# Optimization experiments

Measured on AMD Instinct MI355X. Metric: run time of the kernel, lower is better.

The kernel has to match this reference:

```python
import jax, jax.numpy as jnp
import numpy as np

B, N, D, E_PER, NT, ET, L = 32, 64, 128, 512, 32, 16, 6
E = B * E_PER


def _ln(y, g, b, eps=1e-5):
    m = jnp.mean(y, -1, keepdims=True)
    v = jnp.mean((y - m) ** 2, -1, keepdims=True)
    return (y - m) * jax.lax.rsqrt(v + eps) * g + b


def setup_inputs() -> dict:
    key = jax.random.key(0)
    ks = jax.random.split(key, 40)
    x = jax.random.randint(ks[0], (B * N,), 0, NT)
    src = jax.random.randint(ks[1], (E,), 0, N)
    dst = jax.random.randint(ks[2], (E,), 0, N)
    off = jnp.repeat(jnp.arange(B) * N, E_PER)
    edge_index = jnp.stack([src + off, dst + off])
    edge_attr = jax.random.randint(ks[3], (E,), 0, ET)
    t = jax.random.uniform(ks[4], (B,))

    def lin(k, fi, fo):
        return jax.random.normal(k, (fi, fo), jnp.float32) / np.sqrt(fi).astype(np.float32)

    inp = {
        'x': x, 'edge_index': edge_index, 'edge_attr': edge_attr, 't': t,
        'node_emb': (jax.random.normal(ks[5], (NT, D)) * 0.02).at[0].set(0.0),
        'edge_emb': (jax.random.normal(ks[6], (ET, D)) * 0.02).at[0].set(0.0),
        'temb_W1': lin(ks[7], 1, D), 'temb_b1': jnp.zeros(D),
        'temb_W2': lin(ks[8], D, D), 'temb_b2': jnp.zeros(D),
        'nin_W1': lin(ks[9], D, 2 * D), 'nin_b1': jnp.zeros(2 * D),
        'nin_W2': lin(ks[10], 2 * D, D), 'nin_b2': jnp.zeros(D),
        'ein_W1': lin(ks[11], D, 2 * D), 'ein_b1': jnp.zeros(2 * D),
        'ein_W2': lin(ks[12], 2 * D, D), 'ein_b2': jnp.zeros(D),
        'conv_W1': jax.random.normal(ks[13], (L, 3 * D, D)) / np.sqrt(3 * D).astype(np.float32),
        'conv_b1': jnp.zeros((L, D)),
        'conv_g1': jnp.ones((L, D)), 'conv_bt1': jnp.zeros((L, D)),
        'conv_W2': jax.random.normal(ks[14], (L, D, D)) / np.sqrt(D).astype(np.float32),
        'conv_b2': jnp.zeros((L, D)),
        'conv_g2': jnp.ones((L, D)), 'conv_bt2': jnp.zeros((L, D)),
        'mlp_W1': lin(ks[15], D, D), 'mlp_b1': jnp.zeros(D),
        'mlp_W2': lin(ks[16], D, D), 'mlp_b2': jnp.zeros(D),
        'fn_W1': lin(ks[17], D, 2 * D), 'fn_b1': jnp.zeros(2 * D),
        'fn_W2': lin(ks[18], 2 * D, D), 'fn_b2': jnp.zeros(D),
    }
    return inp


def reference(x, edge_index, edge_attr, t, node_emb, edge_emb,
              temb_W1, temb_b1, temb_W2, temb_b2,
              nin_W1, nin_b1, nin_W2, nin_b2,
              ein_W1, ein_b1, ein_W2, ein_b2,
              conv_W1, conv_b1, conv_g1, conv_bt1,
              conv_W2, conv_b2, conv_g2, conv_bt2,
              mlp_W1, mlp_b1, mlp_W2, mlp_b2,
              fn_W1, fn_b1, fn_W2, fn_b2):
    silu, relu = jax.nn.silu, jax.nn.relu
    # encoders
    h = node_emb[x]                                   # (B*N, D)
    e = edge_emb[edge_attr]                           # (E, D)
    h = relu(h @ nin_W1 + nin_b1) @ nin_W2 + nin_b2
    e = relu(e @ ein_W1 + ein_b1) @ ein_W2 + ein_b2
    # densify (to_dense_adj sums duplicate edges)
    g = edge_index[0] // N
    u = edge_index[0] % N
    v = edge_index[1] % N
    adj = jnp.zeros((B, N, N, D), h.dtype).at[g, u, v].add(e)
    # time embedding scales adj
    tt = silu(silu(t[:, None] @ temb_W1 + temb_b1) @ temb_W2 + temb_b2)  # (B, D)
    X = adj * tt[:, None, None, :]
    A = X  # A fixed to initial masked tensor, X updated residually
    for l in range(L):
        X1 = jnp.einsum('bikd,bkjd->bijd', A, X)      # aggregate over dim 1
        X2 = jnp.einsum('bikd,bkjd->bijd', X, A)      # aggregate over dim 2
        y = jnp.concatenate([X, X1, X2], -1)          # (B,N,N,3D)
        y = relu(_ln(y @ conv_W1[l] + conv_b1[l], conv_g1[l], conv_bt1[l]))
        y = relu(_ln(y @ conv_W2[l] + conv_b2[l], conv_g2[l], conv_bt2[l]))
        X = X + y                                     # residual, samesparse add
    X = X + jnp.transpose(X, (0, 2, 1, 3))
    e_out = X[g, u, v]                                # (E, D) edge gather
    h2 = (silu(X @ mlp_W1 + mlp_b1) @ mlp_W2 + mlp_b2).mean(-2).reshape(B * N, D)
    node_out = relu(h2 @ fn_W1 + fn_b1) @ fn_W2 + fn_b2
    edge_out = relu(e_out @ fn_W1 + fn_b1) @ fn_W2 + fn_b2  # original uses final_layer_node for edges too
    graph_attr = node_out.reshape(B, N, -1).mean(1)   # global mean pool
    return node_out, edge_out, graph_attr
```

## Files before the change

kernel.cpp:

```cpp
#include <hip/hip_runtime.h>
#include <hip/hip_bf16.h>
#include <math.h>

#define NB 32
#define NNODE 64
#define DD 128
#define NSQ 4096
#define EDGES 16384
#define LAYERS 6

typedef __bf16 bf16x8 __attribute__((ext_vector_type(8)));
typedef float f32x4 __attribute__((ext_vector_type(4)));

typedef __attribute__((address_space(1))) const unsigned int g_u32;
typedef __attribute__((address_space(3))) unsigned int l_u32;
__device__ __forceinline__ void gll16(const void* g, void* l){
  __builtin_amdgcn_global_load_lds((g_u32*)g, (l_u32*)l, 16, 0, 0);
}

__device__ __forceinline__ float silu_f(float x){ return x / (1.f + __expf(-x)); }
__device__ __forceinline__ float bf2f(unsigned short h){
  union{unsigned int u; float f;} x; x.u = ((unsigned int)h)<<16; return x.f;
}
__device__ __forceinline__ uint4 addbf8(uint4 a, uint4 b){
  union { __bf16 h[8]; uint4 u; } A, B, O;
  A.u = a; B.u = b;
  #pragma unroll
  for (int e=0;e<8;e++) O.h[e] = (__bf16)((float)A.h[e] + (float)B.h[e]);
  return O.u;
}

__global__ void k_temb(const float* __restrict__ t, const float* __restrict__ W1,
                       const float* __restrict__ b1, const float* __restrict__ W2,
                       const float* __restrict__ b2, float* __restrict__ tt){
  int b = blockIdx.x, d = threadIdx.x;
  __shared__ float h[DD];
  float v = t[b]*W1[d] + b1[d];
  h[d] = silu_f(v);
  __syncthreads();
  float acc = b2[d];
  #pragma unroll 4
  for (int k=0;k<DD;k++) acc = fmaf(h[k], W2[k*DD+d], acc);
  tt[b*DD+d] = silu_f(acc);
}

__global__ void k_edgeenc(const float* __restrict__ emb, const float* __restrict__ W1,
                          const float* __restrict__ b1, const float* __restrict__ W2,
                          const float* __restrict__ b2, float* __restrict__ enc){
  int et = blockIdx.x, tid = threadIdx.x;
  __shared__ float e0[DD];
  __shared__ float hid[2*DD];
  if (tid < DD) e0[tid] = emb[et*DD + tid];
  __syncthreads();
  float a = b1[tid];
  for (int d2=0; d2<DD; d2++) a = fmaf(e0[d2], W1[d2*256 + tid], a);
  hid[tid] = fmaxf(a, 0.f);
  __syncthreads();
  if (tid < DD){
    float o = b2[tid];
    for (int k=0;k<256;k++) o = fmaf(hid[k], W2[k*DD + tid], o);
    enc[et*DD + tid] = o;
  }
}

__global__ void k_cnt(const int* __restrict__ ei, const int* __restrict__ attr,
                      unsigned int* __restrict__ cnt, int b0){
  int e = b0*512 + blockIdx.x*256 + threadIdx.x;
  int s = ei[e], dN = ei[EDGES+e];
  int g = (s>>6) - b0, u = s&63, v = dN&63;
  atomicAdd(&cnt[((size_t)g*4096 + v*64 + u)*16 + attr[e]], 1u);
}

__global__ __launch_bounds__(256) void k_expand(const unsigned int* __restrict__ cnt,
    const float* __restrict__ enc, const float* __restrict__ tt,
    __bf16* __restrict__ A_S, int b0){
  __shared__ float encs[16][128];
  __shared__ float ttl[128];
  __shared__ __bf16 tb[8][256];
  int g = blockIdx.x >> 4;
  int cell0 = (blockIdx.x & 15) << 8;
  int tid = threadIdx.x;
  for (int s = tid; s < 2048; s += 256) encs[s>>7][s&127] = enc[s];
  if (tid < 128) ttl[tid] = tt[(b0+g)*128 + tid];
  unsigned int c16[16];
  { const uint4* src = (const uint4*)(cnt + ((size_t)g*4096 + cell0 + tid)*16);
    uint4 a = src[0], b = src[1], c = src[2], d = src[3];
    c16[0]=a.x; c16[1]=a.y; c16[2]=a.z; c16[3]=a.w;
    c16[4]=b.x; c16[5]=b.y; c16[6]=b.z; c16[7]=b.w;
    c16[8]=c.x; c16[9]=c.y; c16[10]=c.z; c16[11]=c.w;
    c16[12]=d.x; c16[13]=d.y; c16[14]=d.z; c16[15]=d.w; }
  __syncthreads();
  for (int dc=0; dc<16; dc++){
    int d0 = dc*8;
    float vals[8] = {0.f,0.f,0.f,0.f,0.f,0.f,0.f,0.f};
    #pragma unroll
    for (int et=0; et<16; et++){
      unsigned int c = c16[et];
      if (c){
        float fc = (float)c;
        #pragma unroll
        for (int dd=0; dd<8; dd++) vals[dd] = fmaf(fc, encs[et][d0+dd], vals[dd]);
      }
    }
    #pragma unroll
    for (int dd=0; dd<8; dd++) tb[dd][tid] = (__bf16)(vals[dd]*ttl[d0+dd]);
    __syncthreads();
    { int dd = tid>>5, seg = tid&31;
      uint4 v = *(const uint4*)&tb[dd][seg*8];
      *(uint4*)(A_S + ((size_t)(g*128 + d0 + dd)<<12) + cell0 + seg*8) = v; }
    __syncthreads();
  }
}

__global__ __launch_bounds__(256) void k_wprep(const float* __restrict__ W1, const float* __restrict__ W2,
                                               const float* __restrict__ Wm, __bf16* __restrict__ WT){
  int b = blockIdx.x, t = threadIdx.x;
  const float* src; __bf16* dst; int K;
  if (b < 6){ src = W1 + (size_t)b*384*128; dst = WT + (size_t)b*49152; K = 384; }
  else if (b < 12){ src = W2 + (size_t)(b-6)*128*128; dst = WT + 294912 + (size_t)(b-6)*16384; K = 128; }
  else { src = Wm; dst = WT + 393216; K = 128; }
  __shared__ float L[64][129];
  for (int k0 = 0; k0 < K; k0 += 64){
    __syncthreads();
    int r = t>>2, c = (t&3)*32;
    #pragma unroll
    for (int e=0;e<32;e+=4){
      float4 x = *(const float4*)(src + (size_t)(k0+r)*128 + c + e);
      L[r][c+e]=x.x; L[r][c+e+1]=x.y; L[r][c+e+2]=x.z; L[r][c+e+3]=x.w;
    }
    __syncthreads();
    int fo = t>>1, kk = (t&1)*32;
    union { __bf16 h[32]; uint4 u[4]; } o;
    #pragma unroll
    for (int e=0;e<32;e++) o.h[e] = (__bf16)L[kk+e][fo];
    uint4* d4 = (uint4*)(dst + (size_t)fo*K + k0 + kk);
    d4[0]=o.u[0]; d4[1]=o.u[1]; d4[2]=o.u[2]; d4[3]=o.u[3];
  }
}

__global__ __launch_bounds__(256) void k_wprepfn(const float* __restrict__ W1, const float* __restrict__ W2,
                                                 __bf16* __restrict__ o1, __bf16* __restrict__ o2){
  int b = blockIdx.x, t = threadIdx.x;
  const float* src; __bf16* dst; int K, N, k0, n0;
  if (b < 8){ src = W1; dst = o1; K = 128; N = 256; k0 = (b>>2)*64; n0 = (b&3)*64; }
  else { int bb = b-8; src = W2; dst = o2; K = 256; N = 128; k0 = (bb>>1)*64; n0 = (bb&1)*64; }
  __shared__ float L[64][65];
  int r = t>>2, c4 = (t&3)*16;
  #pragma unroll
  for (int e=0;e<16;e+=4){
    float4 x = *(const float4*)(src + (size_t)(k0+r)*N + n0 + c4 + e);
    L[r][c4+e]=x.x; L[r][c4+e+1]=x.y; L[r][c4+e+2]=x.z; L[r][c4+e+3]=x.w;
  }
  __syncthreads();
  int n = t>>2, kc = (t&3)*16;
  union { __bf16 h[16]; uint4 u[2]; } o;
  #pragma unroll
  for (int e=0;e<16;e++) o.h[e] = (__bf16)L[kc+e][n];
  uint4* d4 = (uint4*)(dst + (size_t)(n0+n)*K + k0 + kc);
  d4[0]=o.u[0]; d4[1]=o.u[1];
}

__global__ __launch_bounds__(256) void k_einsum(const __bf16* __restrict__ As,
                                                const __bf16* __restrict__ Xs,
                                                __bf16* __restrict__ X1t, __bf16* __restrict__ X2t){
  __shared__ __bf16 S[8][4096];
  int tid = threadIdx.x;
  int w = tid>>6, lane = tid&63;
  size_t p0 = (size_t)blockIdx.x * 2;
  {
    int slot = (w<2) ? (2+w) : (4+w);
    const __bf16* srcp = ((w<2) ? As : Xs) + (p0 + (w&1))*4096;
    #pragma unroll
    for (int c8 = 0; c8 < 8; c8++){
      int row = c8*8 + (lane>>3);
      int ch  = (lane&7) ^ (row&7);
      gll16(srcp + row*64 + ch*8, (char*)&S[slot][0] + c8*1024);
    }
  }
  __syncthreads();
  {
    int q = tid>>6, v = tid&63;
    int ssl = (q<2) ? (2+q) : (4+q);
    int dsl = (q<2) ? q : (2+q);
    const unsigned char* sb = (const unsigned char*)S[ssl];
    unsigned char* db = (unsigned char*)S[dsl];
    #pragma unroll
    for (int uo=0; uo<8; uo++){
      union { __bf16 h[8]; uint4 u; } pk;
      #pragma unroll
      for (int e=0;e<8;e++){
        int u = uo*8+e;
        pk.h[e] = *(const __bf16*)(sb + u*128 + (((v>>3) ^ (u&7))<<4) + (v&7)*2);
      }
      *(uint4*)(db + v*128 + ((uo ^ (v&7))<<4)) = pk.u;
    }
  }
  __syncthreads();
  int pl = w>>1, pr = w&1;
  const __bf16* M  = pr ? S[4+pl] : S[0+pl];
  const __bf16* Bt = pr ? S[2+pl] : S[6+pl];
  f32x4 acc[4][4];
  #pragma unroll
  for (int a=0;a<4;a++)
    #pragma unroll
    for(int b=0;b<4;b++) acc[a][b] = (f32x4){0.f,0.f,0.f,0.f};
  int lr = lane&15, lq = lane>>4;
  #pragma unroll
  for (int ks=0;ks<2;ks++){
    bf16x8 af[4], bfr[4];
    #pragma unroll
    for (int mt=0;mt<4;mt++){ int r = mt*16+lr; af[mt] = *(const bf16x8*)&M[r*64 + (((ks*4+lq) ^ (r&7))<<3)]; }
    #pragma unroll
    for (int nt=0;nt<4;nt++){ int r = nt*16+lr; bfr[nt] = *(const bf16x8*)&Bt[r*64 + (((ks*4+lq) ^ (r&7))<<3)]; }
    #pragma unroll
    for (int mt=0;mt<4;mt++)
      #pragma unroll
      for (int nt=0;nt<4;nt++)
        acc[mt][nt] = __builtin_amdgcn_mfma_f32_16x16x32_bf16(af[mt], bfr[nt], acc[mt][nt], 0,0,0);
  }
  {
    int dslot = pr ? (4+pl) : pl;
    unsigned char* db = (unsigned char*)&S[dslot][0];
    #pragma unroll
    for (int mt=0;mt<4;mt++)
      #pragma unroll
      for (int nt=0;nt<4;nt++){
        int col = nt*16 + lr; int row0 = mt*16 + lq*4;
        union { __bf16 h[4]; uint2 u; } o;
        #pragma unroll
        for (int r=0;r<4;r++) o.h[r] = (__bf16)acc[mt][nt][r];
        int chunk = row0>>3;
        *(uint2*)(db + col*128 + ((chunk ^ (col&7))<<4) + (row0&7)*2) = o.u;
      }
  }
  __syncthreads();
  #pragma unroll
  for (int s4=0; s4<4; s4++){
    int slot = (s4<2) ? s4 : (2+s4);
    __bf16* dst = ((s4<2) ? X1t : X2t) + (p0 + (s4&1))*4096;
    const unsigned char* sb = (const unsigned char*)&S[slot][0];
    #pragma unroll
    for (int q=0;q<2;q++){
      int t2 = tid + q*256;
      int col = t2>>3, rc = t2&7;
      uint4 v = *(const uint4*)(sb + col*128 + ((rc ^ (col&7))<<4));
      *(uint4*)(dst + t2*8) = v;
    }
  }
}

__global__ __launch_bounds__(256) void k_layer(const __bf16* __restrict__ Xold,
    const __bf16* __restrict__ X1, const __bf16* __restrict__ X2,
    const __bf16* __restrict__ W1t, const __bf16* __restrict__ W2t,
    const float* __restrict__ b1v, const float* __restrict__ g1v, const float* __restrict__ bt1v,
    const float* __restrict__ b2v, const float* __restrict__ g2v, const float* __restrict__ bt2v,
    __bf16* __restrict__ Xnew){
  __shared__ __align__(16) unsigned char RG[32768];
  __shared__ float stats[2][128];
  __bf16* y1T = (__bf16*)RG;
  float (*redS)[128] = (float(*)[128])(RG + 16384);
  float (*redQ)[128] = (float(*)[128])(RG + 18432);
  int tid = threadIdx.x, w = tid>>6, lane = tid&63, lr = lane&15, lq = lane>>4;
  int colTile = blockIdx.x << 7;
  int bl = colTile >> 12;
  int colInB = colTile & 4095;
  int s_fi = tid>>3, s_o = tid&7;
  int r_col = tid>>1;

  f32x4 acc[2][8];
  #pragma unroll
  for (int a=0;a<2;a++)
    #pragma unroll
    for (int b=0;b<8;b++) acc[a][b] = (f32x4){0.f,0.f,0.f,0.f};

#define STAGE(ks, nb) { \
    int gfi = (ks)*32 + s_fi; \
    const __bf16* T = (gfi<128)? Xold : (gfi<256? X1 : X2); \
    int d = gfi & 127; \
    const uint4* src = (const uint4*)(T + ((size_t)(bl*128 + d)<<12) + colInB + s_o*16); \
    uint4 v0 = src[0], v1 = src[1]; \
    unsigned char* Nd = RG + (nb)*8192; \
    *(uint4*)(Nd + s_fi*256 + (((s_o*2+0) ^ (s_fi&15))<<4)) = v0; \
    *(uint4*)(Nd + s_fi*256 + (((s_o*2+1) ^ (s_fi&15))<<4)) = v1; \
  }

#define REPACK(nb) { \
    const unsigned char* Ns = RG + (nb)*8192; \
    unsigned char* Cd = RG + 16384 + (nb)*8192; \
    _Pragma("unroll") \
    for (int j=0;j<2;j++){ \
      int oct = (tid&1)*2 + j; \
      union { __bf16 h[8]; uint4 u; } pk; \
      _Pragma("unroll") \
      for (int e=0;e<8;e++){ \
        int fi = oct*8 + e; \
        pk.h[e] = *(const __bf16*)(Ns + fi*256 + (((r_col>>3) ^ (fi&15))<<4) + (r_col&7)*2); \
      } \
      *(uint4*)(Cd + r_col*64 + ((oct ^ (r_col&3))<<4)) = pk.u; \
    } \
  }

  STAGE(0, 0)
  STAGE(1, 1)
  __syncthreads();
  REPACK(0)
  __syncthreads();

  for (int k=0; k<11; k++){
    int cb = k&1, nb = cb^1;
    const unsigned char* Cc = RG + 16384 + cb*8192;
    bf16x8 af[2];
    #pragma unroll
    for (int mt=0;mt<2;mt++){
      int fo = w*32 + mt*16 + lr;
      af[mt] = *(const bf16x8*)(W1t + (size_t)fo*384 + k*32 + lq*8);
    }
    bf16x8 bfr[8];
    #pragma unroll
    for (int nt=0;nt<8;nt++){ int cr = nt*16+lr; bfr[nt] = *(const bf16x8*)(Cc + cr*64 + ((lq ^ (cr&3))<<4)); }
    #pragma unroll
    for (int mt=0;mt<2;mt++)
      #pragma unroll
      for (int nt=0;nt<8;nt++)
        acc[mt][nt] = __builtin_amdgcn_mfma_f32_16x16x32_bf16(af[mt], bfr[nt], acc[mt][nt], 0,0,0);
    REPACK(nb)
    if (k < 10) STAGE(k+2, cb)
    __syncthreads();
  }
  {
    const unsigned char* Cc = RG + 16384 + 8192;
    bf16x8 af[2];
    #pragma unroll
    for (int mt=0;mt<2;mt++){
      int fo = w*32 + mt*16 + lr;
      af[mt] = *(const bf16x8*)(W1t + (size_t)fo*384 + 11*32 + lq*8);
    }
    bf16x8 bfr[8];
    #pragma unroll
    for (int nt=0;nt<8;nt++){ int cr = nt*16+lr; bfr[nt] = *(const bf16x8*)(Cc + cr*64 + ((lq ^ (cr&3))<<4)); }
    #pragma unroll
    for (int mt=0;mt<2;mt++)
      #pragma unroll
      for (int nt=0;nt<8;nt++)
        acc[mt][nt] = __builtin_amdgcn_mfma_f32_16x16x32_bf16(af[mt], bfr[nt], acc[mt][nt], 0,0,0);
  }

  #pragma unroll
  for (int mt=0;mt<2;mt++){
    #pragma unroll
    for (int r=0;r<4;r++){
      float bv = b1v[w*32 + mt*16 + lq*4 + r];
      #pragma unroll
      for (int nt=0;nt<8;nt++) acc[mt][nt][r] += bv;
    }
  }
  {
    float cs[8], cq[8];
    #pragma unroll
    for (int nt=0;nt<8;nt++){ cs[nt]=0.f; cq[nt]=0.f; }
    #pragma unroll
    for (int mt=0;mt<2;mt++)
      #pragma unroll
      for (int nt=0;nt<8;nt++)
        #pragma unroll
        for (int r=0;r<4;r++){ float v = acc[mt][nt][r]; cs[nt] += v; cq[nt] = fmaf(v,v,cq[nt]); }
    #pragma unroll
    for (int nt=0;nt<8;nt++){
      cs[nt] += __shfl_xor(cs[nt], 16); cq[nt] += __shfl_xor(cq[nt], 16);
      cs[nt] += __shfl_xor(cs[nt], 32); cq[nt] += __shfl_xor(cq[nt], 32);
    }
    if (lq == 0){
      #pragma unroll
      for (int nt=0;nt<8;nt++){ redS[w][nt*16+lr] = cs[nt]; redQ[w][nt*16+lr] = cq[nt]; }
    }
  }
  __syncthreads();
  if (tid < 128){
    float S = redS[0][tid]+redS[1][tid]+redS[2][tid]+redS[3][tid];
    float Q = redQ[0][tid]+redQ[1][tid]+redQ[2][tid]+redQ[3][tid];
    float m = S*(1.f/128.f);
    float var = Q*(1.f/128.f) - m*m;
    stats[0][tid] = m; stats[1][tid] = rsqrtf(var + 1e-5f);
  }
  __syncthreads();
  #pragma unroll
  for (int mt=0;mt<2;mt++){
    int fo1b = w*32 + mt*16 + lq*4;
    float ga[4], be[4];
    #pragma unroll
    for (int r=0;r<4;r++){ ga[r] = g1v[fo1b+r]; be[r] = bt1v[fo1b+r]; }
    #pragma unroll
    for (int nt=0;nt<8;nt++){
      int col = nt*16 + lr;
      union { __bf16 h[4]; uint2 u; } o;
      #pragma unroll
      for (int r=0;r<4;r++){
        float xx = (acc[mt][nt][r] - stats[0][col]) * stats[1][col] * ga[r] + be[r];
        o.h[r] = (__bf16)fmaxf(xx, 0.f);
      }
      *(uint2*)&y1T[col*128 + (fo1b ^ ((col&15)<<3))] = o.u;
    }
  }
  __syncthreads();

  f32x4 acc2[2][8];
  #pragma unroll
  for (int a=0;a<2;a++)
    #pragma unroll
    for (int b=0;b<8;b++) acc2[a][b] = (f32x4){0.f,0.f,0.f,0.f};
  #pragma unroll
  for (int ks2=0; ks2<4; ks2++){
    bf16x8 af[2], bfr[8];
    #pragma unroll
    for (int mt=0;mt<2;mt++){
      int fo = w*32 + mt*16 + lr;
      af[mt] = *(const bf16x8*)(W2t + (size_t)fo*128 + ks2*32 + lq*8);
    }
    #pragma unroll
    for (int nt=0;nt<8;nt++){ int cr = nt*16+lr; bfr[nt] = *(const bf16x8*)&y1T[cr*128 + ((ks2*32 + lq*8) ^ ((cr&15)<<3))]; }
    #pragma unroll
    for (int mt=0;mt<2;mt++)
      #pragma unroll
      for (int nt=0;nt<8;nt++)
        acc2[mt][nt] = __builtin_amdgcn_mfma_f32_16x16x32_bf16(af[mt], bfr[nt], acc2[mt][nt], 0,0,0);
  }
  __syncthreads();

  #pragma unroll
  for (int mt=0;mt<2;mt++){
    #pragma unroll
    for (int r=0;r<4;r++){
      float bv = b2v[w*32 + mt*16 + lq*4 + r];
      #pragma unroll
      for (int nt=0;nt<8;nt++) acc2[mt][nt][r] += bv;
    }
  }
  {
    float cs[8], cq[8];
    #pragma unroll
    for (int nt=0;nt<8;nt++){ cs[nt]=0.f; cq[nt]=0.f; }
    #pragma unroll
    for (int mt=0;mt<2;mt++)
      #pragma unroll
      for (int nt=0;nt<8;nt++)
        #pragma unroll
        for (int r=0;r<4;r++){ float v = acc2[mt][nt][r]; cs[nt] += v; cq[nt] = fmaf(v,v,cq[nt]); }
    #pragma unroll
    for (int nt=0;nt<8;nt++){
      cs[nt] += __shfl_xor(cs[nt], 16); cq[nt] += __shfl_xor(cq[nt], 16);
      cs[nt] += __shfl_xor(cs[nt], 32); cq[nt] += __shfl_xor(cq[nt], 32);
    }
    if (lq == 0){
      #pragma unroll
      for (int nt=0;nt<8;nt++){ redS[w][nt*16+lr] = cs[nt]; redQ[w][nt*16+lr] = cq[nt]; }
    }
  }
  __syncthreads();
  if (tid < 128){
    float S = redS[0][tid]+redS[1][tid]+redS[2][tid]+redS[3][tid];
    float Q = redQ[0][tid]+redQ[1][tid]+redQ[2][tid]+redQ[3][tid];
    float m = S*(1.f/128.f);
    float var = Q*(1.f/128.f) - m*m;
    stats[0][tid] = m; stats[1][tid] = rsqrtf(var + 1e-5f);
  }
  __syncthreads();
  #pragma unroll
  for (int mt=0;mt<2;mt++){
    #pragma unroll
    for (int r=0;r<4;r++){
      int fo = w*32 + mt*16 + lq*4 + r;
      float ga = g2v[fo], be = bt2v[fo];
      size_t rowb = ((size_t)(bl*128 + fo)<<12) + colInB;
      #pragma unroll
      for (int nt=0;nt<8;nt++){
        int cp = nt*16 + lr;
        float xx = (acc2[mt][nt][r] - stats[0][cp]) * stats[1][cp] * ga + be;
        float o = fmaxf(xx, 0.f);
        float old = (float)Xold[rowb + cp];
        Xnew[rowb + cp] = (__bf16)(o + old);
      }
    }
  }
#undef STAGE
#undef REPACK
}

__global__ __launch_bounds__(256) void k_tonm(const __bf16* __restrict__ S, __bf16* __restrict__ NM){
  __shared__ unsigned short L[64][65];
  int b = blockIdx.x;
  int g = b >> 7, dh = (b>>6)&1, cc = b&63;
  int cell0 = cc*64, d0 = dh*64;
  int tid = threadIdx.x;
  int r = tid>>2, c = (tid&3)*16;
  union { unsigned short h[16]; uint4 u[2]; } in;
  const unsigned short* src = (const unsigned short*)S + ((size_t)(g*128 + d0 + r)<<12) + cell0 + c;
  in.u[0] = *(const uint4*)src;
  in.u[1] = *(const uint4*)(src + 8);
  #pragma unroll
  for (int e=0;e<16;e++) L[r][c+e] = in.h[e];
  __syncthreads();
  union { unsigned short h[16]; uint4 u[2]; } o;
  int cr = tid>>2, dc = (tid&3)*16;
  #pragma unroll
  for (int e=0;e<16;e++) o.h[e] = L[dc+e][cr];
  unsigned short* dst = (unsigned short*)NM + (size_t)(g*4096 + cell0 + cr)*128 + d0 + dc;
  *(uint4*)dst       = o.u[0];
  *(uint4*)(dst + 8) = o.u[1];
}

__global__ __launch_bounds__(256) void k_mlph(const __bf16* __restrict__ NM,
    const __bf16* __restrict__ Wt, const float* __restrict__ bias, __bf16* __restrict__ hid){
  __shared__ __align__(16) unsigned char WcB[8192];
  __shared__ __align__(16) unsigned char EcB[8192];
  __bf16* Wc = (__bf16*)WcB;
  unsigned char* Ec = EcB;
  int tid = threadIdx.x, w = tid>>6, lane = tid&63, lr = lane&15, lq = lane>>4;
  int g = blockIdx.x >> 5;
  int cellloc0 = (blockIdx.x & 31) << 7;
  size_t cellbase = ((size_t)g<<12) + cellloc0;
  int mh = w&1, nh = w>>1;
  f32x4 acc[4][4];
  #pragma unroll
  for (int a=0;a<4;a++)
    #pragma unroll
    for (int b=0;b<4;b++) acc[a][b] = (f32x4){0.f,0.f,0.f,0.f};
  for (int ks=0; ks<4; ks++){
    __syncthreads();
    { int fo = tid>>1, half = tid&1;
      const uint4* src = (const uint4*)(Wt + (size_t)fo*128 + ks*32 + half*16);
      uint4 v0 = src[0], v1 = src[1];
      *(uint4*)&Wc[fo*32 + (((half*2+0) ^ (fo&3))<<3)] = v0;
      *(uint4*)&Wc[fo*32 + (((half*2+1) ^ (fo&3))<<3)] = v1;
    }
    { int cell = tid>>1, half = tid&1;
      int cl = cellloc0 + cell;
      int v = cl>>6, u = cl&63;
      size_t cT = ((size_t)g<<12) + u*64 + v;
      const uint4* src  = (const uint4*)(NM + (cellbase + cell)*128 + ks*32 + half*16);
      const uint4* srcT = (const uint4*)(NM + cT*128 + ks*32 + half*16);
      uint4 v0 = addbf8(src[0], srcT[0]);
      uint4 v1 = addbf8(src[1], srcT[1]);
      *(uint4*)(Ec + cell*64 + (((half*2+0) ^ (cell&3))<<4)) = v0;
      *(uint4*)(Ec + cell*64 + (((half*2+1) ^ (cell&3))<<4)) = v1;
    }
    __syncthreads();
    bf16x8 af[4], bfr[4];
    #pragma unroll
    for (int mt=0;mt<4;mt++){ int cr = mh*64 + mt*16 + lr; af[mt] = *(const bf16x8*)(Ec + cr*64 + ((lq ^ (cr&3))<<4)); }
    #pragma unroll
    for (int nt=0;nt<4;nt++){ int fo = nh*64 + nt*16 + lr; bfr[nt] = *(const bf16x8*)&Wc[fo*32 + ((lq ^ (fo&3))<<3)]; }
    #pragma unroll
    for (int mt=0;mt<4;mt++)
      #pragma unroll
      for (int nt=0;nt<4;nt++)
        acc[mt][nt] = __builtin_amdgcn_mfma_f32_16x16x32_bf16(af[mt], bfr[nt], acc[mt][nt], 0,0,0);
  }
  #pragma unroll
  for (int mt=0;mt<4;mt++)
    #pragma unroll
    for (int r=0;r<4;r++){
      size_t cell = cellbase + mh*64 + mt*16 + lq*4 + r;
      #pragma unroll
      for (int nt=0;nt<4;nt++){
        int fo = nh*64 + nt*16 + lr;
        hid[cell*128 + fo] = (__bf16)silu_f(acc[mt][nt][r] + bias[fo]);
      }
    }
}

__global__ void k_ymean(const __bf16* __restrict__ hid, float* __restrict__ ym){
  __shared__ float red[256];
  int g = blockIdx.x >> 6, u = blockIdx.x & 63;
  int fo = threadIdx.x & 127, vh = threadIdx.x >> 7;
  const unsigned short* hu = (const unsigned short*)hid;
  float s = 0.f;
  for (int v = vh; v < 64; v += 2)
    s += bf2f(hu[((size_t)g*4096 + v*64 + u)*128 + fo]);
  red[threadIdx.x] = s;
  __syncthreads();
  if (vh == 0) ym[((size_t)g*64 + u)*128 + fo] = (red[fo] + red[128+fo]) * (1.f/64.f);
}

__global__ void k_h2(const float* __restrict__ ym, const float* __restrict__ W2,
                     const float* __restrict__ b2, float* __restrict__ h2){
  int row = blockIdx.x, fo = threadIdx.x;
  __shared__ float rr[128];
  rr[fo] = ym[(size_t)row*128 + fo];
  __syncthreads();
  float a = b2[fo];
  #pragma unroll 4
  for (int k=0;k<128;k++) a = fmaf(rr[k], W2[k*128+fo], a);
  h2[(size_t)row*128+fo] = a;
}

template<int GATHER>
__global__ __launch_bounds__(256) void k_fmlp(const __bf16* __restrict__ NM, const float* __restrict__ RWS,
    const int* __restrict__ ei,
    const __bf16* __restrict__ W1t, const float* __restrict__ b1,
    const __bf16* __restrict__ W2t, const float* __restrict__ b2,
    float* __restrict__ outp, int b0){
  __shared__ __align__(16) unsigned char RA[32768];
  __shared__ __align__(16) unsigned char RB[8192];
  __shared__ int cells[64];
  __shared__ int cellsT[64];
  __bf16* eo  = (__bf16*)RA;
  __bf16* Wc  = (__bf16*)(RA + 16384);
  __bf16* hid = (__bf16*)RA;
  __bf16* W2c = (__bf16*)RB;
  int tid = threadIdx.x, w = tid>>6, lane = tid&63, lr = lane&15, lq = lane>>4;
  int r0 = blockIdx.x*64;
  if (GATHER){
    if (tid < 64){
      int e = b0*512 + r0 + tid;
      int s = ei[e], dN = ei[EDGES+e];
      int g = (s>>6) - b0, u = s&63, v = dN&63;
      cells[tid]  = g*4096 + v*64 + u;
      cellsT[tid] = g*4096 + u*64 + v;
    }
    __syncthreads();
  }
  { int el = tid>>2, o4 = tid&3;
    if (GATHER){
      const unsigned short* src  = (const unsigned short*)NM + (size_t)cells[el]*128;
      const unsigned short* srcT = (const unsigned short*)NM + (size_t)cellsT[el]*128;
      #pragma unroll
      for (int j=0;j<4;j++){
        int ch = o4*4 + j;
        uint4 v = addbf8(*(const uint4*)(src + ch*8), *(const uint4*)(srcT + ch*8));
        *(uint4*)&eo[el*128 + ((ch*8) ^ ((el&15)*8))] = v;
      }
    } else {
      const float* src = RWS + (size_t)(r0 + el)*128;
      #pragma unroll
      for (int j=0;j<4;j++){
        int ch = o4*4 + j;
        union { __bf16 h[8]; uint4 u; } pk;
        #pragma unroll
        for (int e2=0;e2<8;e2++) pk.h[e2] = (__bf16)src[ch*8 + e2];
        *(uint4*)&eo[el*128 + ((ch*8) ^ ((el&15)*8))] = pk.u;
      }
    }
  }
  f32x4 acc[4][4];
  #pragma unroll
  for (int a=0;a<4;a++)
    #pragma unroll
    for (int b=0;b<4;b++) acc[a][b] = (f32x4){0.f,0.f,0.f,0.f};
  for (int ks=0; ks<4; ks++){
    if (ks) __syncthreads();
    { int fo = tid;
      const uint4* src = (const uint4*)(W1t + (size_t)fo*128 + ks*32);
      #pragma unroll
      for (int o=0;o<4;o++){
        uint4 v = src[o];
        *(uint4*)&Wc[fo*32 + ((o ^ (fo&3))<<3)] = v;
      }
    }
    __syncthreads();
    bf16x8 af[4], bfr[4];
    #pragma unroll
    for (int mt=0;mt<4;mt++){ int fo = w*64+mt*16+lr; af[mt] = *(const bf16x8*)&Wc[fo*32 + ((lq ^ (fo&3))<<3)]; }
    #pragma unroll
    for (int nt=0;nt<4;nt++){ int ed = nt*16+lr; bfr[nt] = *(const bf16x8*)&eo[ed*128 + ((ks*32+lq*8) ^ ((ed&15)*8))]; }
    #pragma unroll
    for (int mt=0;mt<4;mt++)
      #pragma unroll
      for (int nt=0;nt<4;nt++)
        acc[mt][nt] = __builtin_amdgcn_mfma_f32_16x16x32_bf16(af[mt], bfr[nt], acc[mt][nt], 0,0,0);
  }
  __syncthreads();
  #pragma unroll
  for (int mt=0;mt<4;mt++){
    int fob = w*64 + mt*16 + lq*4;
    float bv[4];
    #pragma unroll
    for (int r=0;r<4;r++) bv[r] = b1[fob+r];
    #pragma unroll
    for (int nt=0;nt<4;nt++){
      int ed = nt*16 + lr;
      union { __bf16 h[4]; uint2 u; } o;
      #pragma unroll
      for (int r=0;r<4;r++) o.h[r] = (__bf16)fmaxf(acc[mt][nt][r] + bv[r], 0.f);
      *(uint2*)&hid[ed*256 + (fob ^ ((ed&31)*8))] = o.u;
    }
  }
  f32x4 acc2[4][2];
  #pragma unroll
  for (int a=0;a<4;a++)
    #pragma unroll
    for (int b=0;b<2;b++) acc2[a][b] = (f32x4){0.f,0.f,0.f,0.f};
  int mh = w&1, nh = w>>1;
  for (int ks2=0; ks2<8; ks2++){
    __syncthreads();
    { int fo = tid>>1, half = tid&1;
      const uint4* src = (const uint4*)(W2t + (size_t)fo*256 + ks2*32 + half*16);
      uint4 v0 = src[0], v1 = src[1];
      *(uint4*)&W2c[fo*32 + (((half*2+0) ^ (fo&3))<<3)] = v0;
      *(uint4*)&W2c[fo*32 + (((half*2+1) ^ (fo&3))<<3)] = v1;
    }
    __syncthreads();
    bf16x8 af2[4], bfr2[2];
    #pragma unroll
    for (int mt=0;mt<4;mt++){ int fo2 = mh*64+mt*16+lr; af2[mt] = *(const bf16x8*)&W2c[fo2*32 + ((lq ^ (fo2&3))<<3)]; }
    #pragma unroll
    for (int nt=0;nt<2;nt++){ int ed = nh*32+nt*16+lr; bfr2[nt] = *(const bf16x8*)&hid[ed*256 + ((ks2*32+lq*8) ^ ((ed&31)*8))]; }
    #pragma unroll
    for (int mt=0;mt<4;mt++)
      #pragma unroll
      for (int nt=0;nt<2;nt++)
        acc2[mt][nt] = __builtin_amdgcn_mfma_f32_16x16x32_bf16(af2[mt], bfr2[nt], acc2[mt][nt], 0,0,0);
  }
  #pragma unroll
  for (int mt=0;mt<4;mt++){
    int fo2b = mh*64 + mt*16 + lq*4;
    float bv[4];
    #pragma unroll
    for (int r=0;r<4;r++) bv[r] = b2[fo2b+r];
    #pragma unroll
    for (int nt=0;nt<2;nt++){
      int ed = nh*32 + nt*16 + lr;
      float4 o = make_float4(acc2[mt][nt][0]+bv[0], acc2[mt][nt][1]+bv[1],
                             acc2[mt][nt][2]+bv[2], acc2[mt][nt][3]+bv[3]);
      *(float4*)(outp + (size_t)(r0 + ed)*128 + fo2b) = o;
    }
  }
}

__global__ void k_graph(const float* __restrict__ node_out, float* __restrict__ gout){
  int b = blockIdx.x, d = threadIdx.x;
  float s = 0.f;
  for (int i=0;i<64;i++) s += node_out[(size_t)(b*64+i)*128 + d];
  gout[b*128 + d] = s * (1.f/64.f);
}

extern "C" void kernel_launch(void* const* d_in, const int* in_sizes, int n_in,
                              void* d_out, int out_size, void* d_ws, size_t ws_size,
                              hipStream_t stream) {
  const int*   edge_index = (const int*)d_in[1];
  const int*   edge_attr  = (const int*)d_in[2];
  const float* t        = (const float*)d_in[3];
  const float* edge_emb = (const float*)d_in[5];
  const float* temb_W1  = (const float*)d_in[6];
  const float* temb_b1  = (const float*)d_in[7];
  const float* temb_W2  = (const float*)d_in[8];
  const float* temb_b2  = (const float*)d_in[9];
  const float* ein_W1   = (const float*)d_in[14];
  const float* ein_b1   = (const float*)d_in[15];
  const float* ein_W2   = (const float*)d_in[16];
  const float* ein_b2   = (const float*)d_in[17];
  const float* conv_W1  = (const float*)d_in[18];
  const float* conv_b1  = (const float*)d_in[19];
  const float* conv_g1  = (const float*)d_in[20];
  const float* conv_bt1 = (const float*)d_in[21];
  const float* conv_W2  = (const float*)d_in[22];
  const float* conv_b2  = (const float*)d_in[23];
  const float* conv_g2  = (const float*)d_in[24];
  const float* conv_bt2 = (const float*)d_in[25];
  const float* mlp_W1   = (const float*)d_in[26];
  const float* mlp_b1   = (const float*)d_in[27];
  const float* mlp_W2   = (const float*)d_in[28];
  const float* mlp_b2   = (const float*)d_in[29];
  const float* fn_W1    = (const float*)d_in[30];
  const float* fn_b1    = (const float*)d_in[31];
  const float* fn_W2    = (const float*)d_in[32];
  const float* fn_b2    = (const float*)d_in[33];

  float* ws  = (float*)d_ws;
  float* tt  = ws;
  float* enc = ws + 4096;
  float* ym  = ws + 6144;
  float* h2  = ws + 268288;
  __bf16* WT = (__bf16*)(ws + 530432);
  unsigned int* cnt = (unsigned int*)(ws + 768000);
  const size_t HDRF = 2883584;

  __bf16* fnW1t = WT + 409600;
  __bf16* fnW2t = WT + 442368;

  size_t availF = ws_size / sizeof(float);
  const int cands[6] = {32, 16, 8, 4, 2, 1};
  int C = 1;
  for (int i = 0; i < 6; i++){
    if (HDRF + 4ull * (size_t)cands[i] * 262144ull <= availF){ C = cands[i]; break; }
  }
  const size_t PCB = (size_t)C * 262144;
  __bf16* A_S = (__bf16*)(ws + HDRF);
  __bf16* X_S = (__bf16*)(ws + HDRF + PCB);
  __bf16* X1  = (__bf16*)(ws + HDRF + 2*PCB);
  __bf16* X2  = (__bf16*)(ws + HDRF + 3*PCB);
  float* outf = (float*)d_out;

  k_temb<<<NB, DD, 0, stream>>>(t, temb_W1, temb_b1, temb_W2, temb_b2, tt);
  k_edgeenc<<<16, 256, 0, stream>>>(edge_emb, ein_W1, ein_b1, ein_W2, ein_b2, enc);
  k_wprep<<<13, 256, 0, stream>>>(conv_W1, conv_W2, mlp_W1, WT);
  k_wprepfn<<<16, 256, 0, stream>>>(fn_W1, fn_W2, fnW1t, fnW2t);

  for (int b0 = 0; b0 < NB; b0 += C){
    hipMemsetAsync(cnt, 0, (size_t)C*4096*16*sizeof(unsigned int), stream);
    k_cnt<<<C*2, 256, 0, stream>>>(edge_index, edge_attr, cnt, b0);
    k_expand<<<C*16, 256, 0, stream>>>(cnt, enc, tt, A_S, b0);

    for (int l=0; l<LAYERS; l++){
      const __bf16* Xs_l = (l==0) ? A_S : X_S;
      k_einsum<<<C*64, 256, 0, stream>>>(A_S, Xs_l, X1, X2);
      k_layer<<<C*32, 256, 0, stream>>>(Xs_l, X1, X2,
          WT + (size_t)l*49152, WT + 294912 + (size_t)l*16384,
          conv_b1 + l*DD, conv_g1 + l*DD, conv_bt1 + l*DD,
          conv_b2 + l*DD, conv_g2 + l*DD, conv_bt2 + l*DD, X_S);
    }

    k_tonm<<<C*128, 256, 0, stream>>>(X_S, X1);
    k_mlph<<<C*32, 256, 0, stream>>>(X1, WT + 393216, mlp_b1, X2);
    k_ymean<<<C*64, 256, 0, stream>>>(X2, ym);
    k_h2<<<C*64, 128, 0, stream>>>(ym, mlp_W2, mlp_b2, h2);
    k_fmlp<1><<<C*8, 256, 0, stream>>>(X1, nullptr, edge_index, fnW1t, fn_b1, fnW2t, fn_b2,
                                       outf + 262144 + (size_t)b0*512*128, b0);
    k_fmlp<0><<<C, 256, 0, stream>>>(nullptr, h2, nullptr, fnW1t, fn_b1, fnW2t, fn_b2,
                                     outf + (size_t)b0*64*128, b0);
    k_graph<<<C, DD, 0, stream>>>(outf + (size_t)b0*64*DD, outf + 2359296 + b0*DD);
  }
}
```

Before: 550.3 us.

## Split k_layer work across 8 waves with 512 threads per block

Doubles the k_layer block to 512 threads so each of 8 waves computes a 16-row output slice instead of 32 rows. Staging, repacking and the LayerNorm cross-wave reductions are remapped for the wider block, and redQ moves so the reduction buffers hold 8 partial rows. This halves accumulator registers per thread and adds latency-hiding waves, at the cost of more block-level synchronization participants and the weight A-fragment being loaded by twice as many waves.

```diff
diff --git a/kernel.cpp b/kernel.cpp
--- a/kernel.cpp
+++ b/kernel.cpp
@@ -249,7 +249,7 @@
   }
 }
 
-__global__ __launch_bounds__(256) void k_layer(const __bf16* __restrict__ Xold,
+__global__ __launch_bounds__(512) void k_layer(const __bf16* __restrict__ Xold,
     const __bf16* __restrict__ X1, const __bf16* __restrict__ X2,
     const __bf16* __restrict__ W1t, const __bf16* __restrict__ W2t,
     const float* __restrict__ b1v, const float* __restrict__ g1v, const float* __restrict__ bt1v,
@@ -259,45 +259,38 @@
   __shared__ float stats[2][128];
   __bf16* y1T = (__bf16*)RG;
   float (*redS)[128] = (float(*)[128])(RG + 16384);
-  float (*redQ)[128] = (float(*)[128])(RG + 18432);
+  float (*redQ)[128] = (float(*)[128])(RG + 20480);
   int tid = threadIdx.x, w = tid>>6, lane = tid&63, lr = lane&15, lq = lane>>4;
   int colTile = blockIdx.x << 7;
   int bl = colTile >> 12;
   int colInB = colTile & 4095;
-  int s_fi = tid>>3, s_o = tid&7;
-  int r_col = tid>>1;
-
-  f32x4 acc[2][8];
-  #pragma unroll
-  for (int a=0;a<2;a++)
-    #pragma unroll
-    for (int b=0;b<8;b++) acc[a][b] = (f32x4){0.f,0.f,0.f,0.f};
+  int s_fi = tid>>4, s_o = tid&15;
+  int r_col = tid>>2, r_oct = tid&3;
+  int fo_w = w*16 + lr;
+
+  f32x4 acc[8];
+  #pragma unroll
+  for (int b=0;b<8;b++) acc[b] = (f32x4){0.f,0.f,0.f,0.f};
 
 #define STAGE(ks, nb) { \
     int gfi = (ks)*32 + s_fi; \
     const __bf16* T = (gfi<128)? Xold : (gfi<256? X1 : X2); \
     int d = gfi & 127; \
-    const uint4* src = (const uint4*)(T + ((size_t)(bl*128 + d)<<12) + colInB + s_o*16); \
-    uint4 v0 = src[0], v1 = src[1]; \
+    uint4 v0 = *(const uint4*)(T + ((size_t)(bl*128 + d)<<12) + colInB + s_o*8); \
     unsigned char* Nd = RG + (nb)*8192; \
-    *(uint4*)(Nd + s_fi*256 + (((s_o*2+0) ^ (s_fi&15))<<4)) = v0; \
-    *(uint4*)(Nd + s_fi*256 + (((s_o*2+1) ^ (s_fi&15))<<4)) = v1; \
+    *(uint4*)(Nd + s_fi*256 + ((s_o ^ (s_fi&15))<<4)) = v0; \
   }
 
 #define REPACK(nb) { \
     const unsigned char* Ns = RG + (nb)*8192; \
     unsigned char* Cd = RG + 16384 + (nb)*8192; \
+    union { __bf16 h[8]; uint4 u; } pk; \
     _Pragma("unroll") \
-    for (int j=0;j<2;j++){ \
-      int oct = (tid&1)*2 + j; \
-      union { __bf16 h[8]; uint4 u; } pk; \
-      _Pragma("unroll") \
-      for (int e=0;e<8;e++){ \
-        int fi = oct*8 + e; \
-        pk.h[e] = *(const __bf16*)(Ns + fi*256 + (((r_col>>3) ^ (fi&15))<<4) + (r_col&7)*2); \
-      } \
-      *(uint4*)(Cd + r_col*64 + ((oct ^ (r_col&3))<<4)) = pk.u; \
+    for (int e=0;e<8;e++){ \
+      int fi = r_oct*8 + e; \
+      pk.h[e] = *(const __bf16*)(Ns + fi*256 + (((r_col>>3) ^ (fi&15))<<4) + (r_col&7)*2); \
     } \
+    *(uint4*)(Cd + r_col*64 + ((r_oct ^ (r_col&3))<<4)) = pk.u; \
   }
 
   STAGE(0, 0)
@@ -309,61 +302,42 @@
   for (int k=0; k<11; k++){
     int cb = k&1, nb = cb^1;
     const unsigned char* Cc = RG + 16384 + cb*8192;
-    bf16x8 af[2];
-    #pragma unroll
-    for (int mt=0;mt<2;mt++){
-      int fo = w*32 + mt*16 + lr;
-      af[mt] = *(const bf16x8*)(W1t + (size_t)fo*384 + k*32 + lq*8);
-    }
+    bf16x8 af = *(const bf16x8*)(W1t + (size_t)fo_w*384 + k*32 + lq*8);
     bf16x8 bfr[8];
     #pragma unroll
     for (int nt=0;nt<8;nt++){ int cr = nt*16+lr; bfr[nt] = *(const bf16x8*)(Cc + cr*64 + ((lq ^ (cr&3))<<4)); }
     #pragma unroll
-    for (int mt=0;mt<2;mt++)
-      #pragma unroll
-      for (int nt=0;nt<8;nt++)
-        acc[mt][nt] = __builtin_amdgcn_mfma_f32_16x16x32_bf16(af[mt], bfr[nt], acc[mt][nt], 0,0,0);
+    for (int nt=0;nt<8;nt++)
+      acc[nt] = __builtin_amdgcn_mfma_f32_16x16x32_bf16(af, bfr[nt], acc[nt], 0,0,0);
     REPACK(nb)
     if (k < 10) STAGE(k+2, cb)
     __syncthreads();
   }
   {
     const unsigned char* Cc = RG + 16384 + 8192;
-    bf16x8 af[2];
-    #pragma unroll
-    for (int mt=0;mt<2;mt++){
-      int fo = w*32 + mt*16 + lr;
-      af[mt] = *(const bf16x8*)(W1t + (size_t)fo*384 + 11*32 + lq*8);
-    }
+    bf16x8 af = *(const bf16x8*)(W1t + (size_t)fo_w*384 + 11*32 + lq*8);
     bf16x8 bfr[8];
     #pragma unroll
     for (int nt=0;nt<8;nt++){ int cr = nt*16+lr; bfr[nt] = *(const bf16x8*)(Cc + cr*64 + ((lq ^ (cr&3))<<4)); }
     #pragma unroll
-    for (int mt=0;mt<2;mt++)
-      #pragma unroll
-      for (int nt=0;nt<8;nt++)
-        acc[mt][nt] = __builtin_amdgcn_mfma_f32_16x16x32_bf16(af[mt], bfr[nt], acc[mt][nt], 0,0,0);
-  }
-
-  #pragma unroll
-  for (int mt=0;mt<2;mt++){
-    #pragma unroll
-    for (int r=0;r<4;r++){
-      float bv = b1v[w*32 + mt*16 + lq*4 + r];
-      #pragma unroll
-      for (int nt=0;nt<8;nt++) acc[mt][nt][r] += bv;
-    }
+    for (int nt=0;nt<8;nt++)
+      acc[nt] = __builtin_amdgcn_mfma_f32_16x16x32_bf16(af, bfr[nt], acc[nt], 0,0,0);
+  }
+
+  #pragma unroll
+  for (int r=0;r<4;r++){
+    float bv = b1v[w*16 + lq*4 + r];
+    #pragma unroll
+    for (int nt=0;nt<8;nt++) acc[nt][r] += bv;
   }
   {
     float cs[8], cq[8];
     #pragma unroll
     for (int nt=0;nt<8;nt++){ cs[nt]=0.f; cq[nt]=0.f; }
     #pragma unroll
-    for (int mt=0;mt<2;mt++)
-      #pragma unroll
-      for (int nt=0;nt<8;nt++)
-        #pragma unroll
-        for (int r=0;r<4;r++){ float v = acc[mt][nt][r]; cs[nt] += v; cq[nt] = fmaf(v,v,cq[nt]); }
+    for (int nt=0;nt<8;nt++)
+      #pragma unroll
+      for (int r=0;r<4;r++){ float v = acc[nt][r]; cs[nt] += v; cq[nt] = fmaf(v,v,cq[nt]); }
     #pragma unroll
     for (int nt=0;nt<8;nt++){
       cs[nt] += __shfl_xor(cs[nt], 16); cq[nt] += __shfl_xor(cq[nt], 16);
@@ -376,16 +350,16 @@
   }
   __syncthreads();
   if (tid < 128){
-    float S = redS[0][tid]+redS[1][tid]+redS[2][tid]+redS[3][tid];
-    float Q = redQ[0][tid]+redQ[1][tid]+redQ[2][tid]+redQ[3][tid];
+    float S = 0.f, Q = 0.f;
+    #pragma unroll
+    for (int r2=0;r2<8;r2++){ S += redS[r2][tid]; Q += redQ[r2][tid]; }
     float m = S*(1.f/128.f);
     float var = Q*(1.f/128.f) - m*m;
     stats[0][tid] = m; stats[1][tid] = rsqrtf(var + 1e-5f);
   }
   __syncthreads();
-  #pragma unroll
-  for (int mt=0;mt<2;mt++){
-    int fo1b = w*32 + mt*16 + lq*4;
+  {
+    int fo1b = w*16 + lq*4;
     float ga[4], be[4];
     #pragma unroll
     for (int r=0;r<4;r++){ ga[r] = g1v[fo1b+r]; be[r] = bt1v[fo1b+r]; }
@@ -395,7 +369,7 @@
       union { __bf16 h[4]; uint2 u; } o;
       #pragma unroll
       for (int r=0;r<4;r++){
-        float xx = (acc[mt][nt][r] - stats[0][col]) * stats[1][col] * ga[r] + be[r];
+        float xx = (acc[nt][r] - stats[0][col]) * stats[1][col] * ga[r] + be[r];
         o.h[r] = (__bf16)fmaxf(xx, 0.f);
       }
       *(uint2*)&y1T[col*128 + (fo1b ^ ((col&15)<<3))] = o.u;
@@ -403,48 +377,35 @@
   }
   __syncthreads();
 
-  f32x4 acc2[2][8];
-  #pragma unroll
-  for (int a=0;a<2;a++)
-    #pragma unroll
-    for (int b=0;b<8;b++) acc2[a][b] = (f32x4){0.f,0.f,0.f,0.f};
+  f32x4 acc2[8];
+  #pragma unroll
+  for (int b=0;b<8;b++) acc2[b] = (f32x4){0.f,0.f,0.f,0.f};
   #pragma unroll
   for (int ks2=0; ks2<4; ks2++){
-    bf16x8 af[2], bfr[8];
-    #pragma unroll
-    for (int mt=0;mt<2;mt++){
-      int fo = w*32 + mt*16 + lr;
-      af[mt] = *(const bf16x8*)(W2t + (size_t)fo*128 + ks2*32 + lq*8);
-    }
+    bf16x8 af = *(const bf16x8*)(W2t + (size_t)fo_w*128 + ks2*32 + lq*8);
+    bf16x8 bfr[8];
     #pragma unroll
     for (int nt=0;nt<8;nt++){ int cr = nt*16+lr; bfr[nt] = *(const bf16x8*)&y1T[cr*128 + ((ks2*32 + lq*8) ^ ((cr&15)<<3))]; }
     #pragma unroll
-    for (int mt=0;mt<2;mt++)
-      #pragma unroll
-      for (int nt=0;nt<8;nt++)
-        acc2[mt][nt] = __builtin_amdgcn_mfma_f32_16x16x32_bf16(af[mt], bfr[nt], acc2[mt][nt], 0,0,0);
-  }
-  __syncthreads();
-
-  #pragma unroll
-  for (int mt=0;mt<2;mt++){
-    #pragma unroll
-    for (int r=0;r<4;r++){
-      float bv = b2v[w*32 + mt*16 + lq*4 + r];
-      #pragma unroll
-      for (int nt=0;nt<8;nt++) acc2[mt][nt][r] += bv;
-    }
+    for (int nt=0;nt<8;nt++)
+      acc2[nt] = __builtin_amdgcn_mfma_f32_16x16x32_bf16(af, bfr[nt], acc2[nt], 0,0,0);
+  }
+  __syncthreads();
+
+  #pragma unroll
+  for (int r=0;r<4;r++){
+    float bv = b2v[w*16 + lq*4 + r];
+    #pragma unroll
+    for (int nt=0;nt<8;nt++) acc2[nt][r] += bv;
   }
   {
     float cs[8], cq[8];
     #pragma unroll
     for (int nt=0;nt<8;nt++){ cs[nt]=0.f; cq[nt]=0.f; }
     #pragma unroll
-    for (int mt=0;mt<2;mt++)
-      #pragma unroll
-      for (int nt=0;nt<8;nt++)
-        #pragma unroll
-        for (int r=0;r<4;r++){ float v = acc2[mt][nt][r]; cs[nt] += v; cq[nt] = fmaf(v,v,cq[nt]); }
+    for (int nt=0;nt<8;nt++)
+      #pragma unroll
+      for (int r=0;r<4;r++){ float v = acc2[nt][r]; cs[nt] += v; cq[nt] = fmaf(v,v,cq[nt]); }
     #pragma unroll
     for (int nt=0;nt<8;nt++){
       cs[nt] += __shfl_xor(cs[nt], 16); cq[nt] += __shfl_xor(cq[nt], 16);
@@ -457,28 +418,26 @@
   }
   __syncthreads();
   if (tid < 128){
-    float S = redS[0][tid]+redS[1][tid]+redS[2][tid]+redS[3][tid];
-    float Q = redQ[0][tid]+redQ[1][tid]+redQ[2][tid]+redQ[3][tid];
+    float S = 0.f, Q = 0.f;
+    #pragma unroll
+    for (int r2=0;r2<8;r2++){ S += redS[r2][tid]; Q += redQ[r2][tid]; }
     float m = S*(1.f/128.f);
     float var = Q*(1.f/128.f) - m*m;
     stats[0][tid] = m; stats[1][tid] = rsqrtf(var + 1e-5f);
   }
   __syncthreads();
   #pragma unroll
-  for (int mt=0;mt<2;mt++){
-    #pragma unroll
-    for (int r=0;r<4;r++){
-      int fo = w*32 + mt*16 + lq*4 + r;
-      float ga = g2v[fo], be = bt2v[fo];
-      size_t rowb = ((size_t)(bl*128 + fo)<<12) + colInB;
-      #pragma unroll
-      for (int nt=0;nt<8;nt++){
-        int cp = nt*16 + lr;
-        float xx = (acc2[mt][nt][r] - stats[0][cp]) * stats[1][cp] * ga + be;
-        float o = fmaxf(xx, 0.f);
-        float old = (float)Xold[rowb + cp];
-        Xnew[rowb + cp] = (__bf16)(o + old);
-      }
+  for (int r=0;r<4;r++){
+    int fo = w*16 + lq*4 + r;
+    float ga = g2v[fo], be = bt2v[fo];
+    size_t rowb = ((size_t)(bl*128 + fo)<<12) + colInB;
+    #pragma unroll
+    for (int nt=0;nt<8;nt++){
+      int cp = nt*16 + lr;
+      float xx = (acc2[nt][r] - stats[0][cp]) * stats[1][cp] * ga + be;
+      float o = fmaxf(xx, 0.f);
+      float old = (float)Xold[rowb + cp];
+      Xnew[rowb + cp] = (__bf16)(o + old);
     }
   }
 #undef STAGE
@@ -803,7 +762,7 @@
     for (int l=0; l<LAYERS; l++){
       const __bf16* Xs_l = (l==0) ? A_S : X_S;
       k_einsum<<<C*64, 256, 0, stream>>>(A_S, Xs_l, X1, X2);
-      k_layer<<<C*32, 256, 0, stream>>>(Xs_l, X1, X2,
+      k_layer<<<C*32, 512, 0, stream>>>(Xs_l, X1, X2,
           WT + (size_t)l*49152, WT + 294912 + (size_t)l*16384,
           conv_b1 + l*DD, conv_g1 + l*DD, conv_bt1 + l*DD,
           conv_b2 + l*DD, conv_g2 + l*DD, conv_bt2 + l*DD, X_S);
```

Result: slower. 576.9 us (+4.8%).
